# Optimization experiments

Measured on AMD Instinct MI355X. Metric: run time of the kernel, lower is better.

Reference implementation:

```python
import jax, jax.numpy as jnp
import numpy as np

N_NODES = 10000
N_EDGES = 320000
IN_CH = 128
HID = 64
HEADS = 8
OUT_CH = 2
NEG_SLOPE = 0.2  # PyG GATConv default
EPS = 1e-16      # PyG softmax denominator eps


def setup_inputs() -> dict:
    key = jax.random.key(0)
    ks = jax.random.split(key, 12)
    x = jax.random.normal(ks[0], (N_NODES, IN_CH), dtype=jnp.float32)
    edge_index = jax.random.randint(ks[1], (2, N_EDGES), 0, N_NODES, dtype=jnp.int64)
    s = 0.05
    W1 = jax.random.normal(ks[2], (IN_CH, HEADS * HID), dtype=jnp.float32) * s
    a_src1 = jax.random.normal(ks[3], (HEADS, HID), dtype=jnp.float32) * s
    a_dst1 = jax.random.normal(ks[4], (HEADS, HID), dtype=jnp.float32) * s
    b1 = jnp.zeros((HEADS * HID,), dtype=jnp.float32)
    W2 = jax.random.normal(ks[5], (HEADS * HID, HID), dtype=jnp.float32) * s
    a_src2 = jax.random.normal(ks[6], (1, HID), dtype=jnp.float32) * s
    a_dst2 = jax.random.normal(ks[7], (1, HID), dtype=jnp.float32) * s
    b2 = jnp.zeros((HID,), dtype=jnp.float32)
    Wc = jax.random.normal(ks[8], (HID, OUT_CH), dtype=jnp.float32) * s
    bc = jnp.zeros((OUT_CH,), dtype=jnp.float32)
    return dict(x=x, edge_index=edge_index, W1=W1, a_src1=a_src1, a_dst1=a_dst1,
                b1=b1, W2=W2, a_src2=a_src2, a_dst2=a_dst2, b2=b2, Wc=Wc, bc=bc)


def gat_layer(x, src, dst, W, a_src, a_dst, bias, heads, ch, concat):
    # x: [N, F_in]; src/dst: [E] (self-loops already appended)
    N = x.shape[0]
    h = (x @ W).reshape(N, heads, ch)                 # [N, H, C]
    e_src = jnp.einsum('nhc,hc->nh', h, a_src)        # [N, H]
    e_dst = jnp.einsum('nhc,hc->nh', h, a_dst)
    e = jax.nn.leaky_relu(e_src[src] + e_dst[dst], NEG_SLOPE)  # [E, H]
    # segment softmax over destination nodes (max-shift has zero gradient)
    m = jax.lax.stop_gradient(jax.ops.segment_max(e, dst, num_segments=N))
    w = jnp.exp(e - m[dst])
    denom = jax.ops.segment_sum(w, dst, num_segments=N)
    alpha = w / (denom[dst] + EPS)                    # [E, H]
    # scatter-aggregate weighted source features
    out = jax.ops.segment_sum(h[src] * alpha[:, :, None], dst, num_segments=N)  # [N,H,C]
    out = out.reshape(N, heads * ch) if concat else out.mean(axis=1)
    return out + bias


def reference(x, edge_index, W1, a_src1, a_dst1, b1, W2, a_src2, a_dst2, b2, Wc, bc):
    N = x.shape[0]
    loop = jnp.arange(N, dtype=edge_index.dtype)
    src = jnp.concatenate([edge_index[0], loop])  # PyG add_self_loops=True
    dst = jnp.concatenate([edge_index[1], loop])
    h1 = gat_layer(x, src, dst, W1, a_src1, a_dst1, b1, HEADS, HID, True)
    h1 = jax.nn.elu(h1)
    # dropout is identity in eval mode
    h2 = gat_layer(h1, src, dst, W2, a_src2, a_dst2, b2, 1, HID, False)
    return h2 @ Wc + bc  # [N, 2]
```

## Files before the change

### kernel.cpp

```cpp
#include <hip/hip_runtime.h>
#include <hip/hip_bf16.h>

#define N_NODES 10000
#define N_EDGES 320000
#define IN_CH 128
#define HID 64
#define HEADS 8
#define OUT_CH 2
#define BM 64
#define BK 16
#define ZERO_BLOCKS 16
#define BCAP 128

__device__ __forceinline__ unsigned short f2bf(float f) {
    union { float f; unsigned u; } v; v.f = f;
    unsigned r = (v.u + 0x7FFFu + ((v.u >> 16) & 1u)) >> 16;
    return (unsigned short)r;
}

__global__ __launch_bounds__(256) void gemm1_and_zero(
    const float* __restrict__ A,
    const float* __restrict__ W1,
    const float* __restrict__ a_src1,
    const float* __restrict__ a_dst1,
    unsigned short* __restrict__ hfeatP,
    float* __restrict__ esAll,
    float* __restrict__ edAll,
    int* __restrict__ cursor,
    int M) {
    __shared__ float As[BK][BM + 4];
    __shared__ float Bs[BK][64 + 4];
    int bx = blockIdx.x;
    int tid = threadIdx.x;

    if (bx < ZERO_BLOCKS) {
        for (int i = bx * 256 + tid; i < N_NODES; i += ZERO_BLOCKS * 256)
            cursor[i] = 0;
        return;
    }

    int vb = bx - ZERO_BLOCKS;
    int h  = vb & 7;
    int bm = (vb >> 3) * BM;
    const float* B = W1 + h * 64;
    int tx = tid & 15, ty = tid >> 4;
    int ar = tid >> 2, ac = (tid & 3) * 4;
    int agr = bm + ar;
    int br = tid >> 4, bc = (tid & 15) * 4;
    float4 av, bv;
    av = (agr < M) ? *(const float4*)&A[(size_t)agr * IN_CH + ac]
                   : make_float4(0.f, 0.f, 0.f, 0.f);
    bv = *(const float4*)&B[(size_t)br * (HEADS * HID) + bc];
    float acc[4][4] = {};
    for (int k0 = 0; k0 < IN_CH; k0 += BK) {
        As[ac + 0][ar] = av.x; As[ac + 1][ar] = av.y;
        As[ac + 2][ar] = av.z; As[ac + 3][ar] = av.w;
        *(float4*)&Bs[br][bc] = bv;
        __syncthreads();
        if (k0 + BK < IN_CH) {
            av = (agr < M)
                ? *(const float4*)&A[(size_t)agr * IN_CH + (k0 + BK) + ac]
                : make_float4(0.f, 0.f, 0.f, 0.f);
            bv = *(const float4*)&B[(size_t)(k0 + BK + br) * (HEADS * HID) + bc];
        }
        #pragma unroll
        for (int k = 0; k < BK; k++) {
            float4 a4 = *(const float4*)&As[k][ty * 4];
            float4 b4 = *(const float4*)&Bs[k][tx * 4];
            float a[4] = {a4.x, a4.y, a4.z, a4.w};
            float b[4] = {b4.x, b4.y, b4.z, b4.w};
            #pragma unroll
            for (int i = 0; i < 4; i++)
                #pragma unroll
                for (int j = 0; j < 4; j++) acc[i][j] += a[i] * b[j];
        }
        __syncthreads();
    }
    float asv[4], adv[4];
    #pragma unroll
    for (int j = 0; j < 4; j++) {
        asv[j] = a_src1[h * 64 + tx * 4 + j];
        adv[j] = a_dst1[h * 64 + tx * 4 + j];
    }
    int ph = h >> 1, hs = h & 1;
    #pragma unroll
    for (int i = 0; i < 4; i++) {
        int gr = bm + ty * 4 + i;
        if (gr >= M) continue;
        float sp = 0.f, dp = 0.f;
        ushort4 pk;
        pk.x = f2bf(acc[i][0]); pk.y = f2bf(acc[i][1]);
        pk.z = f2bf(acc[i][2]); pk.w = f2bf(acc[i][3]);
        *(ushort4*)&hfeatP[((size_t)ph * M + gr) * 128 + hs * 64 + tx * 4] = pk;
        #pragma unroll
        for (int j = 0; j < 4; j++) {
            sp += acc[i][j] * asv[j];
            dp += acc[i][j] * adv[j];
        }
        #pragma unroll
        for (int off = 1; off < 16; off <<= 1) {
            sp += __shfl_xor(sp, off, 64);
            dp += __shfl_xor(dp, off, 64);
        }
        if (tx == 0) {
            esAll[(size_t)h * M + gr] = sp;
            edAll[(size_t)h * M + gr] = dp;
        }
    }
}

__global__ void fill_bucket(const int* __restrict__ src,
                            const int* __restrict__ dst, int E,
                            int* cursor, int* __restrict__ bucket) {
    int i = blockIdx.x * blockDim.x + threadIdx.x;
    if (i < E) {
        int d = dst[i];
        int pos = atomicAdd(&cursor[d], 1);
        bucket[(d << 7) + min(pos, BCAP - 1)] = src[i];
    }
}

__global__ __launch_bounds__(256) void gemm2_splitk(
    const float* __restrict__ h1,
    const float* __restrict__ W2,
    float* __restrict__ partial,
    int M) {
    __shared__ float As[BK][BM + 4];
    __shared__ float Bs[BK][64 + 4];
    int tid = threadIdx.x;
    int bm = blockIdx.x * BM;
    int h  = blockIdx.y;
    const float* B = W2 + (size_t)h * 64 * 64;
    float* C = partial + (size_t)h * M * 64;
    int tx = tid & 15, ty = tid >> 4;
    float acc[4][4] = {};
    for (int k0 = 0; k0 < 64; k0 += BK) {
        #pragma unroll
        for (int i = 0; i < 4; i++) {
            int e = tid + i * 256;
            int r = e >> 4, c = e & 15;
            int gr = bm + r;
            As[c][r] = (gr < M)
                ? h1[(size_t)gr * 512 + h * 64 + k0 + c] : 0.f;
        }
        #pragma unroll
        for (int i = 0; i < 4; i++) {
            int e = tid + i * 256;
            int r = e >> 6, c = e & 63;
            Bs[r][c] = B[(size_t)(k0 + r) * 64 + c];
        }
        __syncthreads();
        #pragma unroll
        for (int k = 0; k < BK; k++) {
            float4 a4 = *(const float4*)&As[k][ty * 4];
            float4 b4 = *(const float4*)&Bs[k][tx * 4];
            float a[4] = {a4.x, a4.y, a4.z, a4.w};
            float b[4] = {b4.x, b4.y, b4.z, b4.w};
            #pragma unroll
            for (int i = 0; i < 4; i++)
                #pragma unroll
                for (int j = 0; j < 4; j++) acc[i][j] += a[i] * b[j];
        }
        __syncthreads();
    }
    #pragma unroll
    for (int i = 0; i < 4; i++) {
        int gr = bm + ty * 4 + i;
        if (gr >= M) continue;
        #pragma unroll
        for (int j = 0; j < 4; j++)
            C[(size_t)gr * 64 + tx * 4 + j] = acc[i][j];
    }
}

__global__ __launch_bounds__(256) void gemm2_reduce(
    const float* __restrict__ partial,
    const float* __restrict__ a_src2, const float* __restrict__ a_dst2,
    float* __restrict__ hfeat2, float* __restrict__ es2, float* __restrict__ ed2,
    int M) {
    int n = blockIdx.x * 4 + (threadIdx.x >> 6);
    int l = threadIdx.x & 63;
    if (n >= M) return;
    float v = 0.f;
    #pragma unroll
    for (int h = 0; h < 8; h++)
        v += partial[(size_t)h * M * 64 + (size_t)n * 64 + l];
    hfeat2[(size_t)n * 64 + l] = v;
    float s = v * a_src2[l], t = v * a_dst2[l];
    #pragma unroll
    for (int off = 32; off; off >>= 1) {
        s += __shfl_down(s, off, 64);
        t += __shfl_down(t, off, 64);
    }
    if (l == 0) { es2[n] = s; ed2[n] = t; }
}

__global__ __launch_bounds__(256) void gat_agg_pair(
    const unsigned short* __restrict__ hfeatP, const float* __restrict__ esAll,
    const float* __restrict__ edAll, const int* __restrict__ bucket,
    const int* __restrict__ cursor, const float* __restrict__ b1,
    float* __restrict__ h1, int M) {
    int bx = blockIdx.x;
    int p = bx & 3;
    int n = (bx >> 2) * 4 + (threadIdx.x >> 6);
    int l = threadIdx.x & 63;
    int g = l >> 4;
    int q = l & 15;
    int hq = q >> 3;
    int sub = l & 31;
    int hs = l >> 5;
    int g4 = g << 2;
    int hbaseB = hq << 7;
    const char* hptr = (const char*)hfeatP + (size_t)p * M * 256 + (q << 4);
    const float* esS = esAll + (size_t)(p * 2 + hs) * M;
    float ednS = edAll[(size_t)(p * 2 + hs) * M + n];
    int start = n << 7;
    int deg = min(cursor[n], 96);
    int total = deg + 1;

    float a[8] = {};
    float dloc = 0.f;
    for (int base = 0; base < total; base += 32) {
        int idx = base + sub;
        int sld = bucket[start + idx];
        int sv = (idx < deg) ? sld : n;
        float wgt = 0.f;
        if (idx <= deg) {
            float e = esS[sv] + ednS;
            e = (e > 0.f) ? e : 0.2f * e;
            wgt = __expf(e);
        }
        dloc += wgt;
        int rb = sv << 8;
        int wb = __float_as_int(wgt);
        int cnt = min(32, total - base);
        for (int i = 0; i < cnt; i += 4) {
            int b0 = (i << 2) + g4;
            int rbg = __builtin_amdgcn_ds_bpermute(b0, rb);
            float wg = __int_as_float(
                __builtin_amdgcn_ds_bpermute(b0 + hbaseB, wb));
            const uint4 hv = *(const uint4*)(hptr + rbg);
            a[0] += wg * __uint_as_float(hv.x << 16);
            a[1] += wg * __uint_as_float(hv.x & 0xFFFF0000u);
            a[2] += wg * __uint_as_float(hv.y << 16);
            a[3] += wg * __uint_as_float(hv.y & 0xFFFF0000u);
            a[4] += wg * __uint_as_float(hv.z << 16);
            a[5] += wg * __uint_as_float(hv.z & 0xFFFF0000u);
            a[6] += wg * __uint_as_float(hv.w << 16);
            a[7] += wg * __uint_as_float(hv.w & 0xFFFF0000u);
        }
    }
    #pragma unroll
    for (int off = 16; off; off >>= 1) dloc += __shfl_xor(dloc, off, 64);
    float dother = __shfl_xor(dloc, 32, 64);
    #pragma unroll
    for (int k = 0; k < 8; k++) {
        a[k] += __shfl_xor(a[k], 16, 64);
        a[k] += __shfl_xor(a[k], 32, 64);
    }
    if (g == 0) {
        float d = (hq == 0) ? dloc : dother;
        d += 1e-16f;
        float inv = __builtin_amdgcn_rcpf(d);
        inv = inv * __fmaf_rn(-d, inv, 2.0f);
        const float4 b0v = *(const float4*)&b1[p * 128 + q * 8];
        const float4 b4v = *(const float4*)&b1[p * 128 + q * 8 + 4];
        float vv[8];
        vv[0] = a[0] * inv + b0v.x; vv[1] = a[1] * inv + b0v.y;
        vv[2] = a[2] * inv + b0v.z; vv[3] = a[3] * inv + b0v.w;
        vv[4] = a[4] * inv + b4v.x; vv[5] = a[5] * inv + b4v.y;
        vv[6] = a[6] * inv + b4v.z; vv[7] = a[7] * inv + b4v.w;
        #pragma unroll
        for (int k = 0; k < 8; k++)
            vv[k] = (vv[k] > 0.f) ? vv[k] : (__expf(vv[k]) - 1.f);
        float* dst = &h1[(size_t)n * 512 + p * 128 + q * 8];
        *(float4*)dst = make_float4(vv[0], vv[1], vv[2], vv[3]);
        *(float4*)(dst + 4) = make_float4(vv[4], vv[5], vv[6], vv[7]);
    }
}

__global__ __launch_bounds__(256) void gat_agg2(
    const float* __restrict__ hfeat2, const float* __restrict__ es,
    const float* __restrict__ ed, const int* __restrict__ bucket,
    const int* __restrict__ cursor, const float* __restrict__ b2,
    const float* __restrict__ Wc, const float* __restrict__ bc,
    float* __restrict__ out) {
    int n = blockIdx.x * 4 + (threadIdx.x >> 6);
    int l = threadIdx.x & 63;
    int g = l >> 4;
    int q = l & 15;
    int g4 = g << 2;
    int qoff = q << 4;
    int start = n << 7;
    int deg = min(cursor[n], 96);
    int total = deg + 1;
    float edn = ed[n];

    float ax = 0.f, ay = 0.f, az = 0.f, aw = 0.f;
    float dloc = 0.f;
    for (int base = 0; base < total; base += 64) {
        int cnt = min(64, total - base);
        float wgt = 0.f;
        int sv = n;
        if (l < cnt) {
            int idx = base + l;
            sv = (idx < deg) ? bucket[start + idx] : n;
            float e = es[sv] + edn;
            e = (e > 0.f) ? e : 0.2f * e;
            wgt = __expf(e);
        }
        dloc += wgt;
        int rb = sv << 8;
        int wb = __float_as_int(wgt);
        for (int i = 0; i < cnt; i += 4) {
            int bidx = (i << 2) + g4;
            int rbg = __builtin_amdgcn_ds_bpermute(bidx, rb);
            float wg = __int_as_float(__builtin_amdgcn_ds_bpermute(bidx, wb));
            const float4 hv = *(const float4*)((const char*)hfeat2 + (rbg + qoff));
            ax += wg * hv.x;
            ay += wg * hv.y;
            az += wg * hv.z;
            aw += wg * hv.w;
        }
    }
    float d = dloc;
    #pragma unroll
    for (int off = 32; off; off >>= 1) d += __shfl_down(d, off, 64);
    d = __shfl(d, 0, 64) + 1e-16f;
    float inv = __builtin_amdgcn_rcpf(d);
    inv = inv * __fmaf_rn(-d, inv, 2.0f);
    ax += __shfl_down(ax, 32, 64); ay += __shfl_down(ay, 32, 64);
    az += __shfl_down(az, 32, 64); aw += __shfl_down(aw, 32, 64);
    ax += __shfl_down(ax, 16, 64); ay += __shfl_down(ay, 16, 64);
    az += __shfl_down(az, 16, 64); aw += __shfl_down(aw, 16, 64);
    float p0 = 0.f, p1 = 0.f;
    if (g == 0) {
        const float4 bq = *(const float4*)&b2[q * 4];
        float h0 = ax * inv + bq.x, h1v = ay * inv + bq.y;
        float h2v = az * inv + bq.z, h3 = aw * inv + bq.w;
        const float2* WcV = (const float2*)Wc;
        float2 w0 = WcV[q * 4 + 0], w1 = WcV[q * 4 + 1];
        float2 w2 = WcV[q * 4 + 2], w3 = WcV[q * 4 + 3];
        p0 = h0 * w0.x + h1v * w1.x + h2v * w2.x + h3 * w3.x;
        p1 = h0 * w0.y + h1v * w1.y + h2v * w2.y + h3 * w3.y;
    }
    #pragma unroll
    for (int off = 1; off < 16; off <<= 1) {
        p0 += __shfl_xor(p0, off, 64);
        p1 += __shfl_xor(p1, off, 64);
    }
    if (l == 0) {
        out[n * 2 + 0] = p0 + bc[0];
        out[n * 2 + 1] = p1 + bc[1];
    }
}

extern "C" void kernel_launch(void* const* d_in, const int* in_sizes, int n_in,
                              void* d_out, int out_size, void* d_ws, size_t ws_size,
                              hipStream_t stream) {
    const float* x      = (const float*)d_in[0];
    const int*   eidx   = (const int*)d_in[1];
    const float* W1     = (const float*)d_in[2];
    const float* a_src1 = (const float*)d_in[3];
    const float* a_dst1 = (const float*)d_in[4];
    const float* b1     = (const float*)d_in[5];
    const float* W2     = (const float*)d_in[6];
    const float* a_src2 = (const float*)d_in[7];
    const float* a_dst2 = (const float*)d_in[8];
    const float* b2     = (const float*)d_in[9];
    const float* Wc     = (const float*)d_in[10];
    const float* bc     = (const float*)d_in[11];
    float* out = (float*)d_out;

    const int N = N_NODES, E = N_EDGES;
    const int* esrc = eidx;
    const int* edst = eidx + E;

    size_t off = 0;
    auto alloc = [&](size_t bytes) {
        void* p = (char*)d_ws + off;
        off += (bytes + 255) & ~(size_t)255;
        return p;
    };
    int*   cursor   = (int*)alloc((size_t)N * 4);
    int*   bucket   = (int*)alloc((size_t)N * BCAP * 4);
    unsigned short* hfeatP = (unsigned short*)alloc((size_t)4 * N * 128 * 2);
    float* h1       = (float*)alloc((size_t)N * 512 * 4);
    float* partial  = (float*)alloc((size_t)HEADS * N * 64 * 4);
    float* hfeat2   = (float*)alloc((size_t)N * 64 * 4);
    float* esAll    = (float*)alloc((size_t)HEADS * N * 4);
    float* edAll    = (float*)alloc((size_t)HEADS * N * 4);
    float* es2      = (float*)alloc((size_t)N * 4);
    float* ed2      = (float*)alloc((size_t)N * 4);

    gemm1_and_zero<<<ZERO_BLOCKS + 157 * 8, 256, 0, stream>>>(
        x, W1, a_src1, a_dst1, hfeatP, esAll, edAll, cursor, N);
    fill_bucket<<<(E + 255) / 256, 256, 0, stream>>>(esrc, edst, E, cursor, bucket);
    gat_agg_pair<<<(N / 4) * 4, 256, 0, stream>>>(hfeatP, esAll, edAll,
                                                  bucket, cursor, b1, h1, N);
    dim3 gg2((N + BM - 1) / BM, HEADS);
    gemm2_splitk<<<gg2, 256, 0, stream>>>(h1, W2, partial, N);
    gemm2_reduce<<<(N + 3) / 4, 256, 0, stream>>>(partial, a_src2, a_dst2,
                                                  hfeat2, es2, ed2, N);
    gat_agg2<<<(N + 3) / 4, 256, 0, stream>>>(hfeat2, es2, ed2, bucket, cursor,
                                              b2, Wc, bc, out);
}
```

Measured before the change: 186.3 us.

## Fuse bucket fill into GEMM1 launch and replace split-K reduce with atomics

Zeroing of the cursor and the layer-2 accumulators moves to a single memset, and the edge bucket fill now runs as extra blocks inside the GEMM1 kernel. This removes one launch and lets the atomic bucketing overlap the GEMM. The layer-2 split-K GEMM now accumulates directly into hfeat2, es2 and ed2 with float atomics, which drops the partial buffer and the separate reduce kernel. The cost is atomic contention, with 8 heads adding into each element, and a summation order that is no longer deterministic.

Result: slower. 245.6 us (+31.8%).

```diff
diff --git a/kernel.cpp b/kernel.cpp
--- a/kernel.cpp
+++ b/kernel.cpp
@@ -9,8 +9,9 @@
 #define OUT_CH 2
 #define BM 64
 #define BK 16
-#define ZERO_BLOCKS 16
 #define BCAP 128
+#define FILL_BLOCKS 1250
+#define GEMM1_BLOCKS (157 * 8)
 
 __device__ __forceinline__ unsigned short f2bf(float f) {
     union { float f; unsigned u; } v; v.f = f;
@@ -18,8 +19,9 @@
     return (unsigned short)r;
 }
 
-__global__ __launch_bounds__(256) void gemm1_and_zero(
+__global__ __launch_bounds__(256) void gemm1_and_fill(
     const float* __restrict__ A,
+    const int* __restrict__ esrc, const int* __restrict__ edst,
     const float* __restrict__ W1,
     const float* __restrict__ a_src1,
     const float* __restrict__ a_dst1,
@@ -27,19 +29,22 @@
     float* __restrict__ esAll,
     float* __restrict__ edAll,
     int* __restrict__ cursor,
+    int* __restrict__ bucket,
     int M) {
     __shared__ float As[BK][BM + 4];
     __shared__ float Bs[BK][64 + 4];
     int bx = blockIdx.x;
     int tid = threadIdx.x;
 
-    if (bx < ZERO_BLOCKS) {
-        for (int i = bx * 256 + tid; i < N_NODES; i += ZERO_BLOCKS * 256)
-            cursor[i] = 0;
+    if (bx < FILL_BLOCKS) {
+        int i = bx * 256 + tid;
+        int d = edst[i];
+        int pos = atomicAdd(&cursor[d], 1);
+        bucket[(d << 7) + min(pos, BCAP - 1)] = esrc[i];
         return;
     }
 
-    int vb = bx - ZERO_BLOCKS;
+    int vb = bx - FILL_BLOCKS;
     int h  = vb & 7;
     int bm = (vb >> 3) * BM;
     const float* B = W1 + h * 64;
@@ -109,21 +114,12 @@
     }
 }
 
-__global__ void fill_bucket(const int* __restrict__ src,
-                            const int* __restrict__ dst, int E,
-                            int* cursor, int* __restrict__ bucket) {
-    int i = blockIdx.x * blockDim.x + threadIdx.x;
-    if (i < E) {
-        int d = dst[i];
-        int pos = atomicAdd(&cursor[d], 1);
-        bucket[(d << 7) + min(pos, BCAP - 1)] = src[i];
-    }
-}
-
-__global__ __launch_bounds__(256) void gemm2_splitk(
+__global__ __launch_bounds__(256) void gemm2_splitk_atomic(
     const float* __restrict__ h1,
     const float* __restrict__ W2,
-    float* __restrict__ partial,
+    const float* __restrict__ a_src2, const float* __restrict__ a_dst2,
+    float* __restrict__ hfeat2,
+    float* __restrict__ es2, float* __restrict__ ed2,
     int M) {
     __shared__ float As[BK][BM + 4];
     __shared__ float Bs[BK][64 + 4];
@@ -131,7 +127,6 @@
     int bm = blockIdx.x * BM;
     int h  = blockIdx.y;
     const float* B = W2 + (size_t)h * 64 * 64;
-    float* C = partial + (size_t)h * M * 64;
     int tx = tid & 15, ty = tid >> 4;
     float acc[4][4] = {};
     for (int k0 = 0; k0 < 64; k0 += BK) {
@@ -163,36 +158,33 @@
         }
         __syncthreads();
     }
+    float asv[4], adv[4];
+    #pragma unroll
+    for (int j = 0; j < 4; j++) {
+        asv[j] = a_src2[tx * 4 + j];
+        adv[j] = a_dst2[tx * 4 + j];
+    }
     #pragma unroll
     for (int i = 0; i < 4; i++) {
         int gr = bm + ty * 4 + i;
         if (gr >= M) continue;
-        #pragma unroll
-        for (int j = 0; j < 4; j++)
-            C[(size_t)gr * 64 + tx * 4 + j] = acc[i][j];
-    }
-}
-
-__global__ __launch_bounds__(256) void gemm2_reduce(
-    const float* __restrict__ partial,
-    const float* __restrict__ a_src2, const float* __restrict__ a_dst2,
-    float* __restrict__ hfeat2, float* __restrict__ es2, float* __restrict__ ed2,
-    int M) {
-    int n = blockIdx.x * 4 + (threadIdx.x >> 6);
-    int l = threadIdx.x & 63;
-    if (n >= M) return;
-    float v = 0.f;
-    #pragma unroll
-    for (int h = 0; h < 8; h++)
-        v += partial[(size_t)h * M * 64 + (size_t)n * 64 + l];
-    hfeat2[(size_t)n * 64 + l] = v;
-    float s = v * a_src2[l], t = v * a_dst2[l];
-    #pragma unroll
-    for (int off = 32; off; off >>= 1) {
-        s += __shfl_down(s, off, 64);
-        t += __shfl_down(t, off, 64);
-    }
-    if (l == 0) { es2[n] = s; ed2[n] = t; }
+        float sp = 0.f, dp = 0.f;
+        #pragma unroll
+        for (int j = 0; j < 4; j++) {
+            atomicAdd(&hfeat2[(size_t)gr * 64 + tx * 4 + j], acc[i][j]);
+            sp += acc[i][j] * asv[j];
+            dp += acc[i][j] * adv[j];
+        }
+        #pragma unroll
+        for (int off = 1; off < 16; off <<= 1) {
+            sp += __shfl_xor(sp, off, 64);
+            dp += __shfl_xor(dp, off, 64);
+        }
+        if (tx == 0) {
+            atomicAdd(&es2[gr], sp);
+            atomicAdd(&ed2[gr], dp);
+        }
+    }
 }
 
 __global__ __launch_bounds__(256) void gat_agg_pair(
@@ -372,9 +364,9 @@
     const float* bc     = (const float*)d_in[11];
     float* out = (float*)d_out;
 
-    const int N = N_NODES, E = N_EDGES;
+    const int N = N_NODES;
     const int* esrc = eidx;
-    const int* edst = eidx + E;
+    const int* edst = eidx + N_EDGES;
 
     size_t off = 0;
     auto alloc = [&](size_t bytes) {
@@ -383,25 +375,25 @@
         return p;
     };
     int*   cursor   = (int*)alloc((size_t)N * 4);
+    float* hfeat2   = (float*)alloc((size_t)N * 64 * 4);
+    float* es2      = (float*)alloc((size_t)N * 4);
+    float* ed2      = (float*)alloc((size_t)N * 4);
+    size_t zero_bytes = ((char*)ed2 + (size_t)N * 4) - (char*)cursor;
     int*   bucket   = (int*)alloc((size_t)N * BCAP * 4);
     unsigned short* hfeatP = (unsigned short*)alloc((size_t)4 * N * 128 * 2);
     float* h1       = (float*)alloc((size_t)N * 512 * 4);
-    float* partial  = (float*)alloc((size_t)HEADS * N * 64 * 4);
-    float* hfeat2   = (float*)alloc((size_t)N * 64 * 4);
     float* esAll    = (float*)alloc((size_t)HEADS * N * 4);
     float* edAll    = (float*)alloc((size_t)HEADS * N * 4);
-    float* es2      = (float*)alloc((size_t)N * 4);
-    float* ed2      = (float*)alloc((size_t)N * 4);
-
-    gemm1_and_zero<<<ZERO_BLOCKS + 157 * 8, 256, 0, stream>>>(
-        x, W1, a_src1, a_dst1, hfeatP, esAll, edAll, cursor, N);
-    fill_bucket<<<(E + 255) / 256, 256, 0, stream>>>(esrc, edst, E, cursor, bucket);
+
+    hipMemsetAsync(cursor, 0, zero_bytes, stream);
+    gemm1_and_fill<<<FILL_BLOCKS + GEMM1_BLOCKS, 256, 0, stream>>>(
+        x, esrc, edst, W1, a_src1, a_dst1, hfeatP, esAll, edAll,
+        cursor, bucket, N);
     gat_agg_pair<<<(N / 4) * 4, 256, 0, stream>>>(hfeatP, esAll, edAll,
                                                   bucket, cursor, b1, h1, N);
     dim3 gg2((N + BM - 1) / BM, HEADS);
-    gemm2_splitk<<<gg2, 256, 0, stream>>>(h1, W2, partial, N);
-    gemm2_reduce<<<(N + 3) / 4, 256, 0, stream>>>(partial, a_src2, a_dst2,
-                                                  hfeat2, es2, ed2, N);
+    gemm2_splitk_atomic<<<gg2, 256, 0, stream>>>(h1, W2, a_src2, a_dst2,
+                                                 hfeat2, es2, ed2, N);
     gat_agg2<<<(N + 3) / 4, 256, 0, stream>>>(hfeat2, es2, ed2, bucket, cursor,
                                               b2, Wc, bc, out);
 }
```
